# Kernel optimization log

Measured on AMD Instinct MI355X. Metric: run time of the kernel, lower is better.

## Reference

```python
import jax, jax.numpy as jnp
import numpy as np
import math

B, S, D, H = 2, 4096, 768, 12
HD = D // H  # head_dim = 64


def setup_inputs() -> dict:
    key = jax.random.key(0)
    ks = jax.random.split(key, 12)
    scale = 1.0 / math.sqrt(D)
    inp = {
        "query": jax.random.normal(ks[0], (B, S, D), jnp.float32),
        "key_": jax.random.normal(ks[1], (B, S, D), jnp.float32),
        "value": jax.random.normal(ks[2], (B, S, D), jnp.float32),
        # causal mask: masked_fill where mask == 0
        "mask": jnp.tril(jnp.ones((S, S), jnp.int32))[None, None, :, :],
        "Wq": jax.random.normal(ks[3], (D, D), jnp.float32) * scale,
        "bq": jax.random.normal(ks[4], (D,), jnp.float32) * scale,
        "Wk": jax.random.normal(ks[5], (D, D), jnp.float32) * scale,
        "bk": jax.random.normal(ks[6], (D,), jnp.float32) * scale,
        "Wv": jax.random.normal(ks[7], (D, D), jnp.float32) * scale,
        "bv": jax.random.normal(ks[8], (D,), jnp.float32) * scale,
        "Wo": jax.random.normal(ks[9], (D, D), jnp.float32) * scale,
        "bo": jax.random.normal(ks[10], (D,), jnp.float32) * scale,
    }
    return inp


def reference(query, key_, value, mask, Wq, bq, Wk, bk, Wv, bv, Wo, bo):
    b, s, d = query.shape
    # Linear: x @ W.T + b (torch convention), split heads -> [B, H, S, HD]
    q = (query @ Wq.T + bq).reshape(b, s, H, HD).transpose(0, 2, 1, 3)
    k = (key_ @ Wk.T + bk).reshape(b, s, H, HD).transpose(0, 2, 1, 3)
    v = (value @ Wv.T + bv).reshape(b, s, H, HD).transpose(0, 2, 1, 3)
    # explicit [B, H, S, S] scores as in the source module
    scores = jnp.einsum("bhqd,bhkd->bhqk", q, k) / math.sqrt(HD)
    scores = jnp.where(mask == 0, -jnp.inf, scores)
    attn = jax.nn.softmax(scores, axis=-1)  # dropout p=0.0 -> identity
    out = jnp.einsum("bhqk,bhkd->bhqd", attn, v)
    out = out.transpose(0, 2, 1, 3).reshape(b, s, d)
    return out @ Wo.T + bo
```

## Files before the change

kernel.cpp:

```cpp
#include <hip/hip_runtime.h>

#define Sq 4096
#define Dm 768
#define Hh 12
#define KD 768

typedef short short8 __attribute__((ext_vector_type(8)));
typedef float f32x4 __attribute__((ext_vector_type(4)));
typedef unsigned short bf_t;

__device__ inline bf_t f2bf(float f) {
    unsigned int u = __builtin_bit_cast(unsigned int, f);
    u += 0x7fffu + ((u >> 16) & 1u);
    return (bf_t)(u >> 16);
}

__device__ inline unsigned int pk2bf(float a, float b) {
    unsigned int ua = __builtin_bit_cast(unsigned int, a) + 0x8000u;
    unsigned int ub = __builtin_bit_cast(unsigned int, b) + 0x8000u;
    return __builtin_amdgcn_perm(ub, ua, 0x07060302);
}

__device__ inline float fexp2(float x) {
#if __has_builtin(__builtin_amdgcn_exp2f)
    return __builtin_amdgcn_exp2f(x);
#else
    return exp2f(x);
#endif
}

__device__ inline void gl_lds16(const void* g, void* l) {
    __builtin_amdgcn_global_load_lds(
        (const __attribute__((address_space(1))) unsigned int*)g,
        (__attribute__((address_space(3))) unsigned int*)l, 16, 0, 0);
}

struct CvtJobs { const float* s[8]; bf_t* d[8]; int n[8]; };

__global__ __launch_bounds__(256) void cvt(CvtJobs jobs) {
    const float* s = jobs.s[blockIdx.z];
    bf_t* d = jobs.d[blockIdx.z];
    int n = jobs.n[blockIdx.z];
    int i = (blockIdx.x * 256 + threadIdx.x) * 8;
    if (i < n) {
        float4 a = *(const float4*)(s + i);
        float4 b = *(const float4*)(s + i + 4);
        short8 p;
        p[0] = (short)f2bf(a.x); p[1] = (short)f2bf(a.y);
        p[2] = (short)f2bf(a.z); p[3] = (short)f2bf(a.w);
        p[4] = (short)f2bf(b.x); p[5] = (short)f2bf(b.y);
        p[6] = (short)f2bf(b.z); p[7] = (short)f2bf(b.w);
        *(short8*)(d + i) = p;
    }
}

struct GemmJob {
    const void* __restrict__ A; const bf_t* __restrict__ Bm;
    const float* __restrict__ bias; void* __restrict__ out;
    int mode; float scale; int a32;
};
struct GemmJobs { GemmJob j[3]; };

__global__ __launch_bounds__(256) void gemm_k(GemmJobs jobs) {
    const GemmJob J = jobs.j[blockIdx.z];
    __shared__ bf_t As[128 * 64];
    __shared__ bf_t Bs[128 * 64];
    const int lane = threadIdx.x & 63, wv = threadIdx.x >> 6;
    const int l16 = lane & 15, quad = lane >> 4;
    const int wm = wv >> 1, wn = wv & 1;
    const int m0 = blockIdx.x * 128, n0 = blockIdx.y * 128;

    f32x4 acc[4][4] = {};

    for (int kk = 0; kk < KD; kk += 64) {
        if (J.a32) {
            const float* A32 = (const float*)J.A;
#pragma unroll
            for (int it = 0; it < 4; ++it) {
                int p0 = it * 256 + wv * 64;
                int p = p0 + lane;
                int row = p >> 3;
                int c = (p & 7) ^ (row & 7);
                const float* src = A32 + (size_t)(m0 + row) * KD + kk + c * 8;
                float4 a0 = *(const float4*)src;
                float4 a1 = *(const float4*)(src + 4);
                short8 pp;
                pp[0] = (short)f2bf(a0.x); pp[1] = (short)f2bf(a0.y);
                pp[2] = (short)f2bf(a0.z); pp[3] = (short)f2bf(a0.w);
                pp[4] = (short)f2bf(a1.x); pp[5] = (short)f2bf(a1.y);
                pp[6] = (short)f2bf(a1.z); pp[7] = (short)f2bf(a1.w);
                *(short8*)&As[p * 8] = pp;
                gl_lds16(J.Bm + (size_t)(n0 + row) * KD + kk + c * 8, Bs + p0 * 8);
            }
        } else {
            const bf_t* Ab = (const bf_t*)J.A;
#pragma unroll
            for (int it = 0; it < 4; ++it) {
                int p0 = it * 256 + wv * 64;
                int p = p0 + lane;
                int row = p >> 3;
                int c = (p & 7) ^ (row & 7);
                gl_lds16(Ab + (size_t)(m0 + row) * KD + kk + c * 8, As + p0 * 8);
                gl_lds16(J.Bm + (size_t)(n0 + row) * KD + kk + c * 8, Bs + p0 * 8);
            }
        }
        __syncthreads();
#pragma unroll
        for (int ks = 0; ks < 2; ++ks) {
            short8 a[4], b[4];
#pragma unroll
            for (int i = 0; i < 4; ++i) {
                int row = wm * 64 + i * 16 + l16;
                int pc = (ks * 4 + quad) ^ (row & 7);
                a[i] = *(const short8*)&As[row * 64 + pc * 8];
            }
#pragma unroll
            for (int j = 0; j < 4; ++j) {
                int row = wn * 64 + j * 16 + l16;
                int pc = (ks * 4 + quad) ^ (row & 7);
                b[j] = *(const short8*)&Bs[row * 64 + pc * 8];
            }
#pragma unroll
            for (int i = 0; i < 4; ++i)
#pragma unroll
                for (int j = 0; j < 4; ++j)
                    acc[i][j] = __builtin_amdgcn_mfma_f32_16x16x32_bf16(a[i], b[j], acc[i][j], 0, 0, 0);
        }
        __syncthreads();
    }

#pragma unroll
    for (int i = 0; i < 4; ++i) {
#pragma unroll
        for (int j = 0; j < 4; ++j) {
            int grow = m0 + wm * 64 + i * 16 + quad * 4;
            int gcol = n0 + wn * 64 + j * 16 + l16;
            if (J.mode == 0) {
                float bv = J.bias[gcol];
                int h = gcol >> 6, hd = gcol & 63;
                bf_t* dst = (bf_t*)J.out;
#pragma unroll
                for (int r = 0; r < 4; ++r) {
                    int row = grow + r;
                    int bI = row >> 12, s = row & 4095;
                    dst[(((size_t)(bI * Hh + h) * Sq + s) << 6) + hd] =
                        f2bf((acc[i][j][r] + bv) * J.scale);
                }
            } else if (J.mode == 3) {
                float bv = J.bias[gcol];
                int hh = gcol >> 6, hd = gcol & 63;
                int h2 = hd >> 5, rem = hd & 31, qd = rem >> 3, j2 = rem & 7;
                bf_t* dst = (bf_t*)J.out;
#pragma unroll
                for (int r = 0; r < 4; ++r) {
                    int row = grow + r;
                    int bI = row >> 12, s = row & 4095;
                    int kt2 = s >> 6, rr = s & 63;
                    int g2 = rr >> 5, r5 = rr & 31;
                    int a2 = r5 >> 3, s22 = (r5 >> 2) & 1, b2 = r5 & 3;
                    int lane2 = qd * 16 + (4 * a2 + b2);
                    dst[(size_t)(bI * Hh + hh) * Sq * 64 +
                        kt2 * 4096 + (2 * g2 + s22) * 1024 + h2 * 512 + lane2 * 8 + j2] =
                        f2bf(acc[i][j][r] + bv);
                }
            } else if (J.mode == 4) {
                float bv = J.bias[gcol];
                int hh = gcol >> 6, hd = gcol & 63;
                int ot = hd >> 4, l16v = hd & 15;
                bf_t* dst = (bf_t*)J.out;
#pragma unroll
                for (int r = 0; r < 4; ++r) {
                    int row = grow + r;
                    int bI = row >> 12, s = row & 4095;
                    int kt2 = s >> 6, rr = s & 63;
                    int g2 = rr >> 5, qd = (rr & 31) >> 3, j2 = rr & 7;
                    int lane2 = qd * 16 + l16v;
                    dst[(size_t)(bI * Hh + hh) * Sq * 64 +
                        kt2 * 4096 + (g2 * 4 + ot) * 512 + lane2 * 8 + j2] =
                        f2bf(acc[i][j][r] + bv);
                }
            } else {
                float bv = J.bias[gcol];
                float* dst = (float*)J.out;
#pragma unroll
                for (int r = 0; r < 4; ++r)
                    dst[(size_t)(grow + r) * Dm + gcol] = acc[i][j][r] + bv;
            }
        }
    }
}

#define SHIFT 18.0f
#define NQ 4

__global__ __launch_bounds__(256) void attn(const bf_t* __restrict__ Q,
                                            const bf_t* __restrict__ K,
                                            const bf_t* __restrict__ VT,
                                            bf_t* __restrict__ O) {
    const int id = blockIdx.x + 24 * blockIdx.y;
    const int xcd = id & 7, slot = id >> 3;
    const int bh = xcd * 3 + slot % 3;
    const int qt = 31 - slot / 3;
    const int lane = threadIdx.x & 63, wv = threadIdx.x >> 6;
    const int rg = wv & 1, ksp = wv >> 1;
    const int l16 = lane & 15, quad = lane >> 4;
    const int b = bh / Hh, h = bh % Hh;
    const size_t base = (size_t)bh * Sq * 64;
    const int q0 = qt * 128 + rg * 64;

    __shared__ float ocomb[2][64][68];
    __shared__ float lcomb[2][64];

    const bf_t* __restrict__ Kb = K + base;
    const bf_t* __restrict__ Vb = VT + base;

    short8 qf[NQ][2];
#pragma unroll
    for (int i = 0; i < NQ; ++i) {
        const bf_t* qp = Q + base + (size_t)(q0 + i * 16 + l16) * 64 + quad * 8;
        qf[i][0] = *(const short8*)qp;
        qf[i][1] = *(const short8*)(qp + 32);
    }

    f32x4 oacc[NQ][4] = {};
    f32x4 lsum[NQ] = {};

    const int nkt = (q0 >> 6) + 1;
    const int hsp = (nkt + 1) >> 1;
    const int kt0 = ksp ? hsp : 0;
    const int kt1 = ksp ? nkt : hsp;

    short8 ones32;
#pragma unroll
    for (int j = 0; j < 8; ++j) ones32[j] = (short)0x3F80;

    short8 kf[4][2];
    short8 vfr[4][2];

    int ko = kt0 * 4096 + lane * 8;
    int vo = kt0 * 4096 + lane * 8;

#define LOAD_K()                                                             \
    {                                                                        \
        _Pragma("unroll")                                                    \
        for (int t = 0; t < 4; ++t) {                                        \
            kf[t][0] = *(const short8*)(Kb + ko + t * 1024);                 \
            kf[t][1] = *(const short8*)(Kb + ko + t * 1024 + 512);           \
        }                                                                    \
    }
#define LOAD_V()                                                             \
    {                                                                        \
        _Pragma("unroll")                                                    \
        for (int ot = 0; ot < 4; ++ot)                                       \
            _Pragma("unroll")                                                \
            for (int g = 0; g < 2; ++g)                                      \
                vfr[ot][g] = *(const short8*)(Vb + vo + (g * 4 + ot) * 512); \
    }

    if (kt0 < kt1) { LOAD_K(); LOAD_V(); }

    for (int kt = kt0; kt < kt1; ++kt) {
        const int kv0 = kt * 64;
        const bool more = (kt + 1 < kt1);
#pragma unroll
        for (int i = 0; i < NQ; ++i) {
            f32x4 st[4];
#pragma unroll
            for (int t = 0; t < 4; ++t) {
                f32x4 z = {-SHIFT, -SHIFT, -SHIFT, -SHIFT};
                z = __builtin_amdgcn_mfma_f32_16x16x32_bf16(kf[t][0], qf[i][0], z, 0, 0, 0);
                st[t] = __builtin_amdgcn_mfma_f32_16x16x32_bf16(kf[t][1], qf[i][1], z, 0, 0, 0);
            }
            if (i == NQ - 1) { ko += 4096; if (more) LOAD_K(); }

            alignas(16) unsigned int pkd[4][2];
            const bool need_mask = (kv0 + 63 > q0 + i * 16);
#pragma unroll
            for (int t = 0; t < 4; ++t) {
                int g = t >> 1, s = t & 1;
                f32x4 sv = st[t];
                if (need_mask) {
                    int qrow = q0 + i * 16 + l16;
                    int kb2 = kv0 + 32 * g + 8 * quad + 4 * s;
#pragma unroll
                    for (int r = 0; r < 4; ++r)
                        if (kb2 + r > qrow) sv[r] = -1e30f;
                }
                pkd[t][0] = pk2bf(fexp2(sv[0]), fexp2(sv[1]));
                pkd[t][1] = pk2bf(fexp2(sv[2]), fexp2(sv[3]));
            }
#pragma unroll
            for (int g = 0; g < 2; ++g) {
                short8 pf = *(const short8*)&pkd[2 * g][0];
                lsum[i] = __builtin_amdgcn_mfma_f32_16x16x32_bf16(ones32, pf, lsum[i], 0, 0, 0);
#pragma unroll
                for (int ot = 0; ot < 4; ++ot)
                    oacc[i][ot] = __builtin_amdgcn_mfma_f32_16x16x32_bf16(vfr[ot][g], pf, oacc[i][ot], 0, 0, 0);
            }
        }
        vo += 4096;
        if (more) LOAD_V();
    }
#undef LOAD_K
#undef LOAD_V

    if (ksp) {
#pragma unroll
        for (int i = 0; i < NQ; ++i) {
            int row = i * 16 + l16;
#pragma unroll
            for (int ot = 0; ot < 4; ++ot)
                *(f32x4*)&ocomb[rg][row][ot * 16 + quad * 4] = oacc[i][ot];
            if (quad == 0) lcomb[rg][row] = lsum[i][0];
        }
    }
    __syncthreads();
    if (!ksp) {
#pragma unroll
        for (int i = 0; i < NQ; ++i) {
            int row = i * 16 + l16;
            float ls = lsum[i][0] + lcomb[rg][row];
            float inv = 1.0f / ls;
            int srow = q0 + row;
            bf_t* orow = O + (size_t)(b * Sq + srow) * Dm + h * 64;
#pragma unroll
            for (int ot = 0; ot < 4; ++ot) {
                f32x4 oc = *(const f32x4*)&ocomb[rg][row][ot * 16 + quad * 4];
                uint2 pk;
                pk.x = pk2bf((oacc[i][ot][0] + oc[0]) * inv, (oacc[i][ot][1] + oc[1]) * inv);
                pk.y = pk2bf((oacc[i][ot][2] + oc[2]) * inv, (oacc[i][ot][3] + oc[3]) * inv);
                *(uint2*)(orow + ot * 16 + quad * 4) = pk;
            }
        }
    }
}

extern "C" void kernel_launch(void* const* d_in, const int* in_sizes, int n_in,
                              void* d_out, int out_size, void* d_ws, size_t ws_size,
                              hipStream_t stream) {
    const float* q  = (const float*)d_in[0];
    const float* k  = (const float*)d_in[1];
    const float* v  = (const float*)d_in[2];
    const float* Wq = (const float*)d_in[4];  const float* bq = (const float*)d_in[5];
    const float* Wk = (const float*)d_in[6];  const float* bk = (const float*)d_in[7];
    const float* Wv = (const float*)d_in[8];  const float* bv = (const float*)d_in[9];
    const float* Wo = (const float*)d_in[10]; const float* bo = (const float*)d_in[11];
    float* out = (float*)d_out;

    const float QSCALE = 0.125f * 1.44269504f;

    const size_t NTOK = (size_t)2 * Sq * Dm;
    const size_t NW   = (size_t)Dm * Dm;
    dim3 b256(256);

    bf_t* qb  = (bf_t*)d_ws;
    bf_t* kb  = qb + NTOK;
    bf_t* vb  = kb + NTOK;
    bf_t* ob  = vb + NTOK;
    bf_t* wqb = ob + NTOK;
    bf_t* wkb = wqb + NW;
    bf_t* wvb = wkb + NW;
    bf_t* wob = wvb + NW;

    CvtJobs cw = {{Wq, Wk, Wv, Wo, Wq, Wq, Wq, Wq},
                  {wqb, wkb, wvb, wob, wqb, wqb, wqb, wqb},
                  {(int)NW, (int)NW, (int)NW, (int)NW, 0, 0, 0, 0}};
    cvt<<<dim3(288, 1, 4), b256, 0, stream>>>(cw);

    GemmJobs gp;
    gp.j[0] = {q, wqb, bq, qb, 0, QSCALE, 1};
    gp.j[1] = {k, wkb, bk, kb, 3, 1.0f, 1};
    gp.j[2] = {v, wvb, bv, vb, 4, 1.0f, 1};
    gemm_k<<<dim3(64, 6, 3), b256, 0, stream>>>(gp);

    attn<<<dim3(2 * Hh, Sq / 128), b256, 0, stream>>>(qb, kb, vb, ob);

    GemmJobs go;
    go.j[0] = {ob, wob, bo, out, 2, 1.0f, 0};
    go.j[1] = go.j[0]; go.j[2] = go.j[0];
    gemm_k<<<dim3(64, 6, 1), b256, 0, stream>>>(go);
}
```

Before: 358.8 us.

## Prefetch fp32 A tiles in GEMM and double-buffer K/V fragments in attention

The projection GEMM becomes a template on whether A is fp32. The fp32 A path now loads the next k-slice into registers during the current slice's MFMAs, hiding global load latency behind compute. The attention loop keeps two sets of K/V fragment registers and prefetches two tiles ahead, giving loads more time to land before use. Both changes raise register pressure, which may lower occupancy.

```diff
diff --git a/kernel.cpp b/kernel.cpp
--- a/kernel.cpp
+++ b/kernel.cpp
@@ -57,10 +57,11 @@
 struct GemmJob {
     const void* __restrict__ A; const bf_t* __restrict__ Bm;
     const float* __restrict__ bias; void* __restrict__ out;
-    int mode; float scale; int a32;
+    int mode; float scale;
 };
 struct GemmJobs { GemmJob j[3]; };
 
+template <int A32>
 __global__ __launch_bounds__(256) void gemm_k(GemmJobs jobs) {
     const GemmJob J = jobs.j[blockIdx.z];
     __shared__ bf_t As[128 * 64];
@@ -72,23 +73,36 @@
 
     f32x4 acc[4][4] = {};
 
+    float4 ra[4][2];
+#define LOADA(KK)                                                            \
+    {                                                                        \
+        const float* A32p = (const float*)J.A;                               \
+        _Pragma("unroll")                                                    \
+        for (int it = 0; it < 4; ++it) {                                     \
+            int p = it * 256 + wv * 64 + lane;                               \
+            int row = p >> 3;                                                \
+            int c = (p & 7) ^ (row & 7);                                     \
+            const float* src = A32p + (size_t)(m0 + row) * KD + (KK) + c * 8;\
+            ra[it][0] = *(const float4*)src;                                 \
+            ra[it][1] = *(const float4*)(src + 4);                           \
+        }                                                                    \
+    }
+
+    if (A32) LOADA(0);
+
     for (int kk = 0; kk < KD; kk += 64) {
-        if (J.a32) {
-            const float* A32 = (const float*)J.A;
+        if (A32) {
 #pragma unroll
             for (int it = 0; it < 4; ++it) {
                 int p0 = it * 256 + wv * 64;
                 int p = p0 + lane;
                 int row = p >> 3;
                 int c = (p & 7) ^ (row & 7);
-                const float* src = A32 + (size_t)(m0 + row) * KD + kk + c * 8;
-                float4 a0 = *(const float4*)src;
-                float4 a1 = *(const float4*)(src + 4);
                 short8 pp;
-                pp[0] = (short)f2bf(a0.x); pp[1] = (short)f2bf(a0.y);
-                pp[2] = (short)f2bf(a0.z); pp[3] = (short)f2bf(a0.w);
-                pp[4] = (short)f2bf(a1.x); pp[5] = (short)f2bf(a1.y);
-                pp[6] = (short)f2bf(a1.z); pp[7] = (short)f2bf(a1.w);
+                pp[0] = (short)f2bf(ra[it][0].x); pp[1] = (short)f2bf(ra[it][0].y);
+                pp[2] = (short)f2bf(ra[it][0].z); pp[3] = (short)f2bf(ra[it][0].w);
+                pp[4] = (short)f2bf(ra[it][1].x); pp[5] = (short)f2bf(ra[it][1].y);
+                pp[6] = (short)f2bf(ra[it][1].z); pp[7] = (short)f2bf(ra[it][1].w);
                 *(short8*)&As[p * 8] = pp;
                 gl_lds16(J.Bm + (size_t)(n0 + row) * KD + kk + c * 8, Bs + p0 * 8);
             }
@@ -105,6 +119,7 @@
             }
         }
         __syncthreads();
+        if (A32 && kk + 64 < KD) LOADA(kk + 64);
 #pragma unroll
         for (int ks = 0; ks < 2; ++ks) {
             short8 a[4], b[4];
@@ -128,6 +143,7 @@
         }
         __syncthreads();
     }
+#undef LOADA
 
 #pragma unroll
     for (int i = 0; i < 4; ++i) {
@@ -234,75 +250,79 @@
 #pragma unroll
     for (int j = 0; j < 8; ++j) ones32[j] = (short)0x3F80;
 
-    short8 kf[4][2];
-    short8 vfr[4][2];
-
-    int ko = kt0 * 4096 + lane * 8;
-    int vo = kt0 * 4096 + lane * 8;
-
-#define LOAD_K()                                                             \
+    short8 kfA[4][2], vfrA[4][2];
+    short8 kfB[4][2], vfrB[4][2];
+
+#define LOAD_KF(KF, KT)                                                      \
     {                                                                        \
+        int o = (KT) * 4096 + lane * 8;                                      \
         _Pragma("unroll")                                                    \
         for (int t = 0; t < 4; ++t) {                                        \
-            kf[t][0] = *(const short8*)(Kb + ko + t * 1024);                 \
-            kf[t][1] = *(const short8*)(Kb + ko + t * 1024 + 512);           \
+            KF[t][0] = *(const short8*)(Kb + o + t * 1024);                  \
+            KF[t][1] = *(const short8*)(Kb + o + t * 1024 + 512);            \
         }                                                                    \
     }
-#define LOAD_V()                                                             \
+#define LOAD_VF(VF, KT)                                                      \
     {                                                                        \
+        int o = (KT) * 4096 + lane * 8;                                      \
         _Pragma("unroll")                                                    \
         for (int ot = 0; ot < 4; ++ot)                                       \
             _Pragma("unroll")                                                \
             for (int g = 0; g < 2; ++g)                                      \
-                vfr[ot][g] = *(const short8*)(Vb + vo + (g * 4 + ot) * 512); \
-    }
-
-    if (kt0 < kt1) { LOAD_K(); LOAD_V(); }
-
-    for (int kt = kt0; kt < kt1; ++kt) {
-        const int kv0 = kt * 64;
-        const bool more = (kt + 1 < kt1);
-#pragma unroll
-        for (int i = 0; i < NQ; ++i) {
-            f32x4 st[4];
-#pragma unroll
-            for (int t = 0; t < 4; ++t) {
-                f32x4 z = {-SHIFT, -SHIFT, -SHIFT, -SHIFT};
-                z = __builtin_amdgcn_mfma_f32_16x16x32_bf16(kf[t][0], qf[i][0], z, 0, 0, 0);
-                st[t] = __builtin_amdgcn_mfma_f32_16x16x32_bf16(kf[t][1], qf[i][1], z, 0, 0, 0);
-            }
-            if (i == NQ - 1) { ko += 4096; if (more) LOAD_K(); }
-
-            alignas(16) unsigned int pkd[4][2];
-            const bool need_mask = (kv0 + 63 > q0 + i * 16);
-#pragma unroll
-            for (int t = 0; t < 4; ++t) {
-                int g = t >> 1, s = t & 1;
-                f32x4 sv = st[t];
-                if (need_mask) {
-                    int qrow = q0 + i * 16 + l16;
-                    int kb2 = kv0 + 32 * g + 8 * quad + 4 * s;
-#pragma unroll
-                    for (int r = 0; r < 4; ++r)
-                        if (kb2 + r > qrow) sv[r] = -1e30f;
-                }
-                pkd[t][0] = pk2bf(fexp2(sv[0]), fexp2(sv[1]));
-                pkd[t][1] = pk2bf(fexp2(sv[2]), fexp2(sv[3]));
-            }
-#pragma unroll
-            for (int g = 0; g < 2; ++g) {
-                short8 pf = *(const short8*)&pkd[2 * g][0];
-                lsum[i] = __builtin_amdgcn_mfma_f32_16x16x32_bf16(ones32, pf, lsum[i], 0, 0, 0);
-#pragma unroll
-                for (int ot = 0; ot < 4; ++ot)
-                    oacc[i][ot] = __builtin_amdgcn_mfma_f32_16x16x32_bf16(vfr[ot][g], pf, oacc[i][ot], 0, 0, 0);
-            }
-        }
-        vo += 4096;
-        if (more) LOAD_V();
-    }
-#undef LOAD_K
-#undef LOAD_V
+                VF[ot][g] = *(const short8*)(Vb + o + (g * 4 + ot) * 512);   \
+    }
+
+#define TILE_BODY(KF, VF, KT)                                                \
+    {                                                                        \
+        const int kv0 = (KT) * 64;                                           \
+        _Pragma("unroll")                                                    \
+        for (int i = 0; i < NQ; ++i) {                                       \
+            f32x4 st[4];                                                     \
+            _Pragma("unroll")                                                \
+            for (int t = 0; t < 4; ++t) {                                    \
+                f32x4 z = {-SHIFT, -SHIFT, -SHIFT, -SHIFT};                  \
+                z = __builtin_amdgcn_mfma_f32_16x16x32_bf16(KF[t][0], qf[i][0], z, 0, 0, 0); \
+                st[t] = __builtin_amdgcn_mfma_f32_16x16x32_bf16(KF[t][1], qf[i][1], z, 0, 0, 0); \
+            }                                                                \
+            if (i == NQ - 1 && (KT) + 2 < kt1) LOAD_KF(KF, (KT) + 2);        \
+            alignas(16) unsigned int pkd[4][2];                              \
+            const bool need_mask = (kv0 + 63 > q0 + i * 16);                 \
+            _Pragma("unroll")                                                \
+            for (int t = 0; t < 4; ++t) {                                    \
+                int g = t >> 1, s = t & 1;                                   \
+                f32x4 sv = st[t];                                            \
+                if (need_mask) {                                             \
+                    int qrow = q0 + i * 16 + l16;                            \
+                    int kb2 = kv0 + 32 * g + 8 * quad + 4 * s;               \
+                    _Pragma("unroll")                                        \
+                    for (int r = 0; r < 4; ++r)                              \
+                        if (kb2 + r > qrow) sv[r] = -1e30f;                  \
+                }                                                            \
+                pkd[t][0] = pk2bf(fexp2(sv[0]), fexp2(sv[1]));               \
+                pkd[t][1] = pk2bf(fexp2(sv[2]), fexp2(sv[3]));               \
+            }                                                                \
+            _Pragma("unroll")                                                \
+            for (int g = 0; g < 2; ++g) {                                    \
+                short8 pf = *(const short8*)&pkd[2 * g][0];                  \
+                lsum[i] = __builtin_amdgcn_mfma_f32_16x16x32_bf16(ones32, pf, lsum[i], 0, 0, 0); \
+                _Pragma("unroll")                                            \
+                for (int ot = 0; ot < 4; ++ot)                               \
+                    oacc[i][ot] = __builtin_amdgcn_mfma_f32_16x16x32_bf16(VF[ot][g], pf, oacc[i][ot], 0, 0, 0); \
+            }                                                                \
+        }                                                                    \
+        if ((KT) + 2 < kt1) LOAD_VF(VF, (KT) + 2);                           \
+    }
+
+    if (kt0 < kt1)     { LOAD_KF(kfA, kt0);     LOAD_VF(vfrA, kt0); }
+    if (kt0 + 1 < kt1) { LOAD_KF(kfB, kt0 + 1); LOAD_VF(vfrB, kt0 + 1); }
+
+    for (int kt = kt0; kt < kt1; kt += 2) {
+        TILE_BODY(kfA, vfrA, kt);
+        if (kt + 1 < kt1) TILE_BODY(kfB, vfrB, kt + 1);
+    }
+#undef LOAD_KF
+#undef LOAD_VF
+#undef TILE_BODY
 
     if (ksp) {
 #pragma unroll
@@ -368,15 +388,15 @@
     cvt<<<dim3(288, 1, 4), b256, 0, stream>>>(cw);
 
     GemmJobs gp;
-    gp.j[0] = {q, wqb, bq, qb, 0, QSCALE, 1};
-    gp.j[1] = {k, wkb, bk, kb, 3, 1.0f, 1};
-    gp.j[2] = {v, wvb, bv, vb, 4, 1.0f, 1};
-    gemm_k<<<dim3(64, 6, 3), b256, 0, stream>>>(gp);
+    gp.j[0] = {q, wqb, bq, qb, 0, QSCALE};
+    gp.j[1] = {k, wkb, bk, kb, 3, 1.0f};
+    gp.j[2] = {v, wvb, bv, vb, 4, 1.0f};
+    gemm_k<1><<<dim3(64, 6, 3), b256, 0, stream>>>(gp);
 
     attn<<<dim3(2 * Hh, Sq / 128), b256, 0, stream>>>(qb, kb, vb, ob);
 
     GemmJobs go;
-    go.j[0] = {ob, wob, bo, out, 2, 1.0f, 0};
+    go.j[0] = {ob, wob, bo, out, 2, 1.0f};
     go.j[1] = go.j[0]; go.j[2] = go.j[0];
-    gemm_k<<<dim3(64, 6, 1), b256, 0, stream>>>(go);
-}
+    gemm_k<0><<<dim3(64, 6, 1), b256, 0, stream>>>(go);
+}
```

After: 341.9 us, median of 2. 1.05x faster.
